# Kernel optimization log

Hardware: AMD Instinct MI355X
Metric: run time of the kernel (lower is better)

## Reference

```python
import jax, jax.numpy as jnp
import numpy as np

DIM = 128
HEADS = 32
DIM_HEAD = 64
INNER = DIM * DIM_HEAD  # 8192, as written in the source (dim * dim_head)
D = INNER // HEADS      # 256 per-head dim
B, N = 1, 2048
ROT = 64                # partial rotary width (l)
SCALE = DIM ** (-0.5)   # source uses dim**-0.5, not head-dim


def _rotate_half(x):
    # x: [..., l]; split as (j d) with j=2 -> cat(-x2, x1)
    x1, x2 = jnp.split(x, 2, axis=-1)
    return jnp.concatenate((-x2, x1), axis=-1)


def _apply_rotary(q, k, freqs):
    # freqs: [n, l]; q,k: [b,h,n,d] with l <= d (partial rotary)
    l = freqs.shape[-1]
    cos, sin = jnp.cos(freqs), jnp.sin(freqs)  # broadcast over b,h
    ql, qr = q[..., :l], q[..., l:]
    kl, kr = k[..., :l], k[..., l:]
    ql = ql * cos + _rotate_half(ql) * sin
    kl = kl * cos + _rotate_half(kl) * sin
    return jnp.concatenate((ql, qr), axis=-1), jnp.concatenate((kl, kr), axis=-1)


def setup_inputs() -> dict:
    key = jax.random.key(0)
    k1, k2, k3, k4, k5 = jax.random.split(key, 5)
    return {
        "x": jax.random.normal(k1, (B, N, DIM), dtype=jnp.float32),
        "Wqkv": jax.random.normal(k2, (3 * INNER, DIM), dtype=jnp.float32) * 0.02,
        "Wproj": jax.random.normal(k3, (DIM, INNER), dtype=jnp.float32) * 0.02,
        "bproj": jax.random.normal(k4, (DIM,), dtype=jnp.float32) * 0.02,
        "rotary_pos_emb": jax.random.normal(k5, (N, ROT), dtype=jnp.float32),
    }


def reference(x, Wqkv, Wproj, bproj, rotary_pos_emb):
    b, n, _ = x.shape
    qkv = x @ Wqkv.T                                   # [b, n, 3*inner]
    qkv = qkv.reshape(b, n, 3, HEADS, D)               # (qkv h d) ordering
    qkv = jnp.transpose(qkv, (2, 0, 3, 1, 4))          # [3, b, h, n, d]
    q, k, v = qkv[0], qkv[1], qkv[2]
    q, k = _apply_rotary(q, k, rotary_pos_emb)
    energy = jnp.einsum("bhid,bhjd->bhij", q, k) * SCALE  # [b,h,n,n]
    attn = jax.nn.softmax(energy, axis=-1)
    out = jnp.einsum("bhij,bhjd->bhid", attn, v)       # [b,h,n,d]
    out = jnp.transpose(out, (0, 2, 1, 3)).reshape(b, n, INNER)
    return out @ Wproj.T + bproj
```

## Files before the change

### kernel.cpp

```cpp
#include <hip/hip_runtime.h>


typedef unsigned short u16;
typedef unsigned int u32;
typedef __attribute__((ext_vector_type(8))) u16 u16x8;
typedef __attribute__((ext_vector_type(8))) __bf16 bf16x8;
typedef __attribute__((ext_vector_type(4))) float f32x4;
typedef __attribute__((ext_vector_type(16))) float f32x16;
typedef __attribute__((ext_vector_type(4))) u32 u32x4;
typedef __attribute__((ext_vector_type(2))) u32 u32x2;

#define DEV static __device__ __forceinline__

DEV u16 f2b(float f) {
  __bf16 h = (__bf16)f;
  return __builtin_bit_cast(u16, h);
}
DEV float b2f(u16 b) {
  u32 u = ((u32)b) << 16;
  return __builtin_bit_cast(float, u);
}
DEV u32 pk2(float a, float b) { return (u32)f2b(a) | ((u32)f2b(b) << 16); }

DEV f32x4 mfma16(u16x8 a, u16x8 b, f32x4 c) {
  return __builtin_amdgcn_mfma_f32_16x16x32_bf16(
      __builtin_bit_cast(bf16x8, a), __builtin_bit_cast(bf16x8, b), c, 0, 0, 0);
}
DEV f32x16 mfma32(u16x8 a, u16x8 b, f32x16 c) {
  return __builtin_amdgcn_mfma_f32_32x32x16_bf16(
      __builtin_bit_cast(bf16x8, a), __builtin_bit_cast(bf16x8, b), c, 0, 0, 0);
}

DEV int swz(int row, int kelem, int rowBytes) {
  return row * rowBytes + ((kelem * 2) ^ ((row & 7) << 4));
}

DEV void dma16(const void* g, void* l) {
  __builtin_amdgcn_global_load_lds(
      (const __attribute__((address_space(1))) void*)g,
      (__attribute__((address_space(3))) void*)l, 16, 0, 0);
}

__global__ __launch_bounds__(256) void k_cvt(const float* __restrict__ src,
                                             u16* __restrict__ dst, int n8) {
  int i = blockIdx.x * 256 + threadIdx.x;
  if (i >= n8) return;
  const float4* s = (const float4*)src;
  float4 a = s[i * 2], b = s[i * 2 + 1];
  u16x8 o;
  o[0] = f2b(a.x); o[1] = f2b(a.y); o[2] = f2b(a.z); o[3] = f2b(a.w);
  o[4] = f2b(b.x); o[5] = f2b(b.y); o[6] = f2b(b.z); o[7] = f2b(b.w);
  *(u16x8*)(dst + (size_t)i * 8) = o;
}

__global__ __launch_bounds__(256) void k_qkv(const u16* __restrict__ xb,
                                             const u16* __restrict__ wb,
                                             u16* __restrict__ qw,
                                             u16* __restrict__ kw,
                                             u16* __restrict__ vw) {
  __shared__ char lds[65536];
  const int tid = threadIdx.x;
  const int rt = blockIdx.x % 192, nt = blockIdx.x / 192;
  const int r0 = rt * 128, n0 = nt * 128;
#pragma unroll
  for (int p = 0; p < 8; ++p) {
    int row = p * 16 + (tid >> 4);
    int k0 = (tid & 15) * 8;
    *(u16x8*)(lds + swz(row, k0, 256)) =
        *(const u16x8*)(wb + (size_t)(r0 + row) * 128 + k0);
    *(u16x8*)(lds + 32768 + swz(row, k0, 256)) =
        *(const u16x8*)(xb + (size_t)(n0 + row) * 128 + k0);
  }
  __syncthreads();
  const int wid = tid >> 6, lane = tid & 63, lq = lane & 15, g = lane >> 4;
  const int wr = wid >> 1, wn = wid & 1;
  const bool isV = (r0 >= 16384);
  f32x4 acc[4][4] = {};
#pragma unroll
  for (int ks = 0; ks < 4; ++ks) {
    u16x8 wa[4], xa[4];
#pragma unroll
    for (int i = 0; i < 4; ++i) {
      int rw = wr * 64 + i * 16 + lq;
      wa[i] = *(const u16x8*)(lds + swz(rw, ks * 32 + g * 8, 256));
      int rx = wn * 64 + i * 16 + lq;
      xa[i] = *(const u16x8*)(lds + 32768 + swz(rx, ks * 32 + g * 8, 256));
    }
    if (!isV) {
#pragma unroll
      for (int i = 0; i < 4; ++i)
#pragma unroll
        for (int j = 0; j < 4; ++j) acc[i][j] = mfma16(wa[i], xa[j], acc[i][j]);
    } else {
#pragma unroll
      for (int i = 0; i < 4; ++i)
#pragma unroll
        for (int j = 0; j < 4; ++j) acc[i][j] = mfma16(xa[j], wa[i], acc[i][j]);
    }
  }
  const float SMQ = 0.08838834764831845f * 1.4426950408889634f;
  if (!isV) {
#pragma unroll
    for (int i = 0; i < 4; ++i) {
      int rb = r0 + wr * 64 + i * 16 + g * 4;
      u16* dst0 = (rb >= 8192) ? kw : qw;
      float scl = (rb >= 8192) ? 1.0f : SMQ;
      int hd = rb & 8191;
      int h = hd >> 8, db = hd & 255;
#pragma unroll
      for (int j = 0; j < 4; ++j) {
        int n = n0 + wn * 64 + j * 16 + lq;
        u32x2 pk;
        pk.x = pk2(acc[i][j][0] * scl, acc[i][j][1] * scl);
        pk.y = pk2(acc[i][j][2] * scl, acc[i][j][3] * scl);
        *(u32x2*)(dst0 + ((size_t)h * 2048 + n) * 256 + db) = pk;
      }
    }
  } else {
#pragma unroll
    for (int i = 0; i < 4; ++i) {
      int rc = r0 - 16384 + wr * 64 + i * 16 + lq;
      int h = rc >> 8, d = rc & 255;
#pragma unroll
      for (int j = 0; j < 4; ++j) {
        int nb = n0 + wn * 64 + j * 16 + g * 4;
        u32x2 pk;
        pk.x = pk2(acc[i][j][0], acc[i][j][1]);
        pk.y = pk2(acc[i][j][2], acc[i][j][3]);
        *(u32x2*)(vw + ((size_t)h * 256 + d) * 2048 + nb) = pk;
      }
    }
  }
}

__global__ __launch_bounds__(256) void k_rope(u16* __restrict__ qw,
                                              u16* __restrict__ kw,
                                              const float* __restrict__ fr) {
  int idx = blockIdx.x * 256 + threadIdx.x;
  int seg = idx & 3;
  int n = (idx >> 2) & 2047;
  int h = (idx >> 13) & 31;
  u16* base = ((idx >> 18) ? kw : qw) + ((size_t)h * 2048 + n) * 256 + seg * 8;
  u16x8 lo = *(const u16x8*)base;
  u16x8 hi = *(const u16x8*)(base + 32);
  const float* f = fr + n * 64 + seg * 8;
  u16x8 nlo, nhi;
#pragma unroll
  for (int e = 0; e < 8; ++e) {
    float fl = f[e], fh = f[e + 32];
    float sl, cl, sh, ch;
    __sincosf(fl, &sl, &cl);
    __sincosf(fh, &sh, &ch);
    float a = b2f(lo[e]), b = b2f(hi[e]);
    nlo[e] = f2b(a * cl - b * sl);
    nhi[e] = f2b(b * ch + a * sh);
  }
  *(u16x8*)base = nlo;
  *(u16x8*)(base + 32) = nhi;
}

__global__ __launch_bounds__(256, 2) void k_attn(const u16* __restrict__ qw,
                                                 const u16* __restrict__ kw,
                                                 const u16* __restrict__ vw,
                                                 u16* __restrict__ ow) {
  __shared__ char lds[65536];
  const int tid = threadIdx.x;
  const int h = blockIdx.x & 31;
  const int qb = blockIdx.x >> 5;
  const int wid = tid >> 6, lane = tid & 63;
  const int l31 = lane & 31, h2 = lane >> 5;
  const int q0w = qb * 128 + wid * 32;
  const int lane16 = lane * 16;

  const u16* kbase = kw + (size_t)h * 2048 * 256;
  const u16* vbase = vw + (size_t)h * 256 * 2048;

  int koff[4], voff[4];
  {
    int c0 = l31 & 3, hh = (l31 >> 2) & 1, c1 = l31 >> 3;
    int gkv = 16 * (c1 >> 1) + 8 * hh + 4 * (c1 & 1) + c0;
#pragma unroll
    for (int i = 0; i < 4; ++i) {
      int s = wid * 4 + i;
      koff[i] = gkv * 256 + s * 16 + h2 * 8;
      voff[i] = ((s >> 1) * 32 + l31) * 2048 + (s & 1) * 16 + h2 * 8;
    }
  }

  u16x8 qf[16];
  {
    const u16* qp = qw + ((size_t)h * 2048 + q0w + l31) * 256 + h2 * 8;
#pragma unroll
    for (int dt = 0; dt < 16; ++dt) qf[dt] = *(const u16x8*)(qp + dt * 16);
  }

  f32x16 oacc[8] = {};
  float lrun = 0.f;

#define STAGE(T, BUF)                                                 \
  {                                                                   \
    const int kv0_ = (T) * 32;                                        \
    char* b_ = lds + (BUF) * 32768;                                   \
    _Pragma("unroll") for (int i = 0; i < 4; ++i) {                   \
      dma16(kbase + (size_t)kv0_ * 256 + koff[i],                     \
            b_ + (wid * 4 + i) * 1024);                               \
      dma16(vbase + kv0_ + voff[i],                                   \
            b_ + 16384 + (wid * 4 + i) * 1024);                       \
    }                                                                 \
  }

  STAGE(0, 0);

  for (int t = 0; t < 64; ++t) {
    asm volatile("s_waitcnt vmcnt(0)" ::: "memory");
    __builtin_amdgcn_s_barrier();
    asm volatile("" ::: "memory");
    if (t < 63) STAGE(t + 1, (t + 1) & 1);

    const char* kb = lds + (t & 1) * 32768;

    f32x16 sA = {}, sB = {};
    __builtin_amdgcn_s_setprio(1);
#pragma unroll
    for (int dt = 0; dt < 16; dt += 2) {
      u16x8 ka0 = *(const u16x8*)(kb + dt * 1024 + lane16);
      sA = mfma32(ka0, qf[dt], sA);
      u16x8 ka1 = *(const u16x8*)(kb + (dt + 1) * 1024 + lane16);
      sB = mfma32(ka1, qf[dt + 1], sB);
    }
    __builtin_amdgcn_s_setprio(0);

    float p[16];
#pragma unroll
    for (int r = 0; r < 16; ++r)
      p[r] = __builtin_amdgcn_exp2f(sA[r] + sB[r]);
    float s8[8];
#pragma unroll
    for (int r = 0; r < 8; ++r) s8[r] = p[r] + p[r + 8];
#pragma unroll
    for (int r = 0; r < 4; ++r) s8[r] = s8[r] + s8[r + 4];
    lrun += (s8[0] + s8[1]) + (s8[2] + s8[3]);

    u32x4 b0v, b1v;
#pragma unroll
    for (int w = 0; w < 4; ++w) {
      b0v[w] = pk2(p[2 * w], p[2 * w + 1]);
      b1v[w] = pk2(p[8 + 2 * w], p[9 + 2 * w]);
    }
    u16x8 pb0 = __builtin_bit_cast(u16x8, b0v);
    u16x8 pb1 = __builtin_bit_cast(u16x8, b1v);

    const char* vb = kb + 16384;
    __builtin_amdgcn_s_setprio(1);
#pragma unroll
    for (int dt = 0; dt < 8; ++dt) {
      u16x8 v0 = *(const u16x8*)(vb + (dt * 2) * 1024 + lane16);
      oacc[dt] = mfma32(v0, pb0, oacc[dt]);
      u16x8 v1 = *(const u16x8*)(vb + (dt * 2 + 1) * 1024 + lane16);
      oacc[dt] = mfma32(v1, pb1, oacc[dt]);
    }
    __builtin_amdgcn_s_setprio(0);
  }
#undef STAGE

  lrun += __shfl_xor(lrun, 32);
  float inv = 1.0f / lrun;
  u16* orow = ow + (size_t)(q0w + l31) * 8192 + h * 256 + h2 * 4;
#pragma unroll
  for (int dt = 0; dt < 8; ++dt)
#pragma unroll
    for (int k = 0; k < 4; ++k) {
      u32x2 o2;
      o2.x = pk2(oacc[dt][4 * k] * inv, oacc[dt][4 * k + 1] * inv);
      o2.y = pk2(oacc[dt][4 * k + 2] * inv, oacc[dt][4 * k + 3] * inv);
      *(u32x2*)(orow + dt * 32 + k * 8) = o2;
    }
}

__global__ __launch_bounds__(256) void k_proj(const u16* __restrict__ ow,
                                              const u16* __restrict__ wp,
                                              float* __restrict__ part) {
  __shared__ char lds[49152];
  const int tid = threadIdx.x;
  const int nt = blockIdx.x >> 3, kc = blockIdx.x & 7;
  const int n0 = nt * 64, kb = kc * 1024;
  const int wid = tid >> 6, lane = tid & 63, lq = lane & 15, g = lane >> 4;
  f32x4 acc[8] = {};
  for (int kt = 0; kt < 8; ++kt) {
    int kk = kb + kt * 128;
#pragma unroll
    for (int p = 0; p < 4; ++p) {
      int nr = p * 16 + (tid >> 4);
      int k0 = (tid & 15) * 8;
      *(u16x8*)(lds + swz(nr, k0, 256)) =
          *(const u16x8*)(ow + (size_t)(n0 + nr) * 8192 + kk + k0);
    }
#pragma unroll
    for (int p = 0; p < 8; ++p) {
      int er = p * 16 + (tid >> 4);
      int k0 = (tid & 15) * 8;
      *(u16x8*)(lds + 16384 + swz(er, k0, 256)) =
          *(const u16x8*)(wp + (size_t)er * 8192 + kk + k0);
    }
    __syncthreads();
#pragma unroll
    for (int ks = 0; ks < 4; ++ks) {
      int nr = wid * 16 + lq;
      u16x8 oa = *(const u16x8*)(lds + swz(nr, ks * 32 + g * 8, 256));
#pragma unroll
      for (int ef = 0; ef < 8; ++ef) {
        int er = ef * 16 + lq;
        u16x8 wf = *(const u16x8*)(lds + 16384 + swz(er, ks * 32 + g * 8, 256));
        acc[ef] = mfma16(oa, wf, acc[ef]);
      }
    }
    __syncthreads();
  }
  float* pb = part + (size_t)kc * 262144;
#pragma unroll
  for (int ef = 0; ef < 8; ++ef)
#pragma unroll
    for (int r = 0; r < 4; ++r) {
      int n = n0 + wid * 16 + g * 4 + r;
      pb[n * 128 + ef * 16 + lq] = acc[ef][r];
    }
}

__global__ __launch_bounds__(256) void k_reduce(const float* __restrict__ part,
                                                const float* __restrict__ bias,
                                                float* __restrict__ out) {
  int i = blockIdx.x * 256 + threadIdx.x;
  float s = bias[i & 127];
#pragma unroll
  for (int c = 0; c < 8; ++c) s += part[(size_t)c * 262144 + i];
  out[i] = s;
}

extern "C" void kernel_launch(void* const* d_in, const int* in_sizes, int n_in,
                              void* d_out, int out_size, void* d_ws, size_t ws_size,
                              hipStream_t stream) {
  const float* x = (const float*)d_in[0];
  const float* wqkv = (const float*)d_in[1];
  const float* wproj = (const float*)d_in[2];
  const float* bproj = (const float*)d_in[3];
  const float* rope = (const float*)d_in[4];
  char* ws = (char*)d_ws;
  u16* xb    = (u16*)(ws);
  u16* wqkvb = (u16*)(ws + 524288);
  u16* wpb   = (u16*)(ws + 6815744);
  u16* qw    = (u16*)(ws + 8912896);
  u16* kw    = (u16*)(ws + 42467328);
  u16* vw    = (u16*)(ws + 76021760);
  u16* owv   = (u16*)(ws + 109576192);
  float* part = (float*)(ws + 8912896);

  k_cvt<<<128, 256, 0, stream>>>(x, xb, 32768);
  k_cvt<<<1536, 256, 0, stream>>>(wqkv, wqkvb, 393216);
  k_cvt<<<512, 256, 0, stream>>>(wproj, wpb, 131072);
  k_qkv<<<3072, 256, 0, stream>>>(xb, wqkvb, qw, kw, vw);
  k_rope<<<2048, 256, 0, stream>>>(qw, kw, rope);
  k_attn<<<512, 256, 0, stream>>>(qw, kw, vw, owv);
  k_proj<<<256, 256, 0, stream>>>(owv, wpb, part);
  k_reduce<<<1024, 256, 0, stream>>>(part, bproj, (float*)d_out);
}
```

Baseline: 240.4 us.

## Process two query tiles per wave in attention to reuse K/V fragments

Each wave now handles 64 query rows as two 32-row chunks, so every K and V fragment read from LDS feeds two MFMAs instead of one. The grid is halved to 256 blocks and launch bounds drop to one block per CU to allow the doubled Q and accumulator register footprint. The aim is to cut LDS reads and global K/V staging traffic per unit of compute. The cost is much higher register pressure and lower occupancy, and 256 blocks may underfill the 256 CUs' latency hiding.

```diff
diff --git a/kernel.cpp b/kernel.cpp
--- a/kernel.cpp
+++ b/kernel.cpp
@@ -159,7 +159,7 @@
   *(u16x8*)(base + 32) = nhi;
 }
 
-__global__ __launch_bounds__(256, 2) void k_attn(const u16* __restrict__ qw,
+__global__ __launch_bounds__(256, 1) void k_attn(const u16* __restrict__ qw,
                                                  const u16* __restrict__ kw,
                                                  const u16* __restrict__ vw,
                                                  u16* __restrict__ ow) {
@@ -169,7 +169,7 @@
   const int qb = blockIdx.x >> 5;
   const int wid = tid >> 6, lane = tid & 63;
   const int l31 = lane & 31, h2 = lane >> 5;
-  const int q0w = qb * 128 + wid * 32;
+  const int q0w = qb * 256 + wid * 64;
   const int lane16 = lane * 16;
 
   const u16* kbase = kw + (size_t)h * 2048 * 256;
@@ -187,15 +187,17 @@
     }
   }
 
-  u16x8 qf[16];
-  {
-    const u16* qp = qw + ((size_t)h * 2048 + q0w + l31) * 256 + h2 * 8;
-#pragma unroll
-    for (int dt = 0; dt < 16; ++dt) qf[dt] = *(const u16x8*)(qp + dt * 16);
-  }
-
-  f32x16 oacc[8] = {};
-  float lrun = 0.f;
+  u16x8 qf[2][16];
+#pragma unroll
+  for (int c = 0; c < 2; ++c) {
+    const u16* qp =
+        qw + ((size_t)h * 2048 + q0w + c * 32 + l31) * 256 + h2 * 8;
+#pragma unroll
+    for (int dt = 0; dt < 16; ++dt) qf[c][dt] = *(const u16x8*)(qp + dt * 16);
+  }
+
+  f32x16 oa0[8] = {}, oa1[8] = {};
+  float lrun0 = 0.f, lrun1 = 0.f;
 
 #define STAGE(T, BUF)                                                 \
   {                                                                   \
@@ -219,61 +221,88 @@
 
     const char* kb = lds + (t & 1) * 32768;
 
-    f32x16 sA = {}, sB = {};
+    f32x16 s0 = {}, s1 = {};
     __builtin_amdgcn_s_setprio(1);
 #pragma unroll
-    for (int dt = 0; dt < 16; dt += 2) {
-      u16x8 ka0 = *(const u16x8*)(kb + dt * 1024 + lane16);
-      sA = mfma32(ka0, qf[dt], sA);
-      u16x8 ka1 = *(const u16x8*)(kb + (dt + 1) * 1024 + lane16);
-      sB = mfma32(ka1, qf[dt + 1], sB);
+    for (int dt = 0; dt < 16; ++dt) {
+      u16x8 ka = *(const u16x8*)(kb + dt * 1024 + lane16);
+      s0 = mfma32(ka, qf[0][dt], s0);
+      s1 = mfma32(ka, qf[1][dt], s1);
     }
     __builtin_amdgcn_s_setprio(0);
 
-    float p[16];
-#pragma unroll
-    for (int r = 0; r < 16; ++r)
-      p[r] = __builtin_amdgcn_exp2f(sA[r] + sB[r]);
-    float s8[8];
-#pragma unroll
-    for (int r = 0; r < 8; ++r) s8[r] = p[r] + p[r + 8];
-#pragma unroll
-    for (int r = 0; r < 4; ++r) s8[r] = s8[r] + s8[r + 4];
-    lrun += (s8[0] + s8[1]) + (s8[2] + s8[3]);
-
-    u32x4 b0v, b1v;
-#pragma unroll
-    for (int w = 0; w < 4; ++w) {
-      b0v[w] = pk2(p[2 * w], p[2 * w + 1]);
-      b1v[w] = pk2(p[8 + 2 * w], p[9 + 2 * w]);
-    }
-    u16x8 pb0 = __builtin_bit_cast(u16x8, b0v);
-    u16x8 pb1 = __builtin_bit_cast(u16x8, b1v);
+    u16x8 pb00, pb01, pb10, pb11;
+    {
+      float p[16];
+#pragma unroll
+      for (int r = 0; r < 16; ++r) p[r] = __builtin_amdgcn_exp2f(s0[r]);
+      float t8[8];
+#pragma unroll
+      for (int r = 0; r < 8; ++r) t8[r] = p[r] + p[r + 8];
+#pragma unroll
+      for (int r = 0; r < 4; ++r) t8[r] = t8[r] + t8[r + 4];
+      lrun0 += (t8[0] + t8[1]) + (t8[2] + t8[3]);
+      u32x4 b0v, b1v;
+#pragma unroll
+      for (int w = 0; w < 4; ++w) {
+        b0v[w] = pk2(p[2 * w], p[2 * w + 1]);
+        b1v[w] = pk2(p[8 + 2 * w], p[9 + 2 * w]);
+      }
+      pb00 = __builtin_bit_cast(u16x8, b0v);
+      pb01 = __builtin_bit_cast(u16x8, b1v);
+    }
+    {
+      float p[16];
+#pragma unroll
+      for (int r = 0; r < 16; ++r) p[r] = __builtin_amdgcn_exp2f(s1[r]);
+      float t8[8];
+#pragma unroll
+      for (int r = 0; r < 8; ++r) t8[r] = p[r] + p[r + 8];
+#pragma unroll
+      for (int r = 0; r < 4; ++r) t8[r] = t8[r] + t8[r + 4];
+      lrun1 += (t8[0] + t8[1]) + (t8[2] + t8[3]);
+      u32x4 b0v, b1v;
+#pragma unroll
+      for (int w = 0; w < 4; ++w) {
+        b0v[w] = pk2(p[2 * w], p[2 * w + 1]);
+        b1v[w] = pk2(p[8 + 2 * w], p[9 + 2 * w]);
+      }
+      pb10 = __builtin_bit_cast(u16x8, b0v);
+      pb11 = __builtin_bit_cast(u16x8, b1v);
+    }
 
     const char* vb = kb + 16384;
     __builtin_amdgcn_s_setprio(1);
 #pragma unroll
     for (int dt = 0; dt < 8; ++dt) {
       u16x8 v0 = *(const u16x8*)(vb + (dt * 2) * 1024 + lane16);
-      oacc[dt] = mfma32(v0, pb0, oacc[dt]);
+      oa0[dt] = mfma32(v0, pb00, oa0[dt]);
+      oa1[dt] = mfma32(v0, pb10, oa1[dt]);
       u16x8 v1 = *(const u16x8*)(vb + (dt * 2 + 1) * 1024 + lane16);
-      oacc[dt] = mfma32(v1, pb1, oacc[dt]);
+      oa0[dt] = mfma32(v1, pb01, oa0[dt]);
+      oa1[dt] = mfma32(v1, pb11, oa1[dt]);
     }
     __builtin_amdgcn_s_setprio(0);
   }
 #undef STAGE
 
-  lrun += __shfl_xor(lrun, 32);
-  float inv = 1.0f / lrun;
-  u16* orow = ow + (size_t)(q0w + l31) * 8192 + h * 256 + h2 * 4;
+  lrun0 += __shfl_xor(lrun0, 32);
+  lrun1 += __shfl_xor(lrun1, 32);
+  float inv0 = 1.0f / lrun0, inv1 = 1.0f / lrun1;
+  u16* orow0 = ow + (size_t)(q0w + l31) * 8192 + h * 256 + h2 * 4;
+  u16* orow1 = orow0 + 32 * 8192;
 #pragma unroll
   for (int dt = 0; dt < 8; ++dt)
 #pragma unroll
     for (int k = 0; k < 4; ++k) {
       u32x2 o2;
-      o2.x = pk2(oacc[dt][4 * k] * inv, oacc[dt][4 * k + 1] * inv);
-      o2.y = pk2(oacc[dt][4 * k + 2] * inv, oacc[dt][4 * k + 3] * inv);
-      *(u32x2*)(orow + dt * 32 + k * 8) = o2;
+      o2.x = pk2(oa0[dt][4 * k] * inv0, oa0[dt][4 * k + 1] * inv0);
+      o2.y = pk2(oa0[dt][4 * k + 2] * inv0, oa0[dt][4 * k + 3] * inv0);
+      *(u32x2*)(orow0 + dt * 32 + k * 8) = o2;
+      u32x2 o3;
+      o3.x = pk2(oa1[dt][4 * k] * inv1, oa1[dt][4 * k + 1] * inv1);
+      o3.y = pk2(oa1[dt][4 * k + 2] * inv1, oa1[dt][4 * k + 3] * inv1);
+      *(u32x2*)(orow1 + dt * 32 + k * 8) = o3;
     }
 }
 
@@ -359,7 +388,7 @@
   k_cvt<<<512, 256, 0, stream>>>(wproj, wpb, 131072);
   k_qkv<<<3072, 256, 0, stream>>>(xb, wqkvb, qw, kw, vw);
   k_rope<<<2048, 256, 0, stream>>>(qw, kw, rope);
-  k_attn<<<512, 256, 0, stream>>>(qw, kw, vw, owv);
+  k_attn<<<256, 256, 0, stream>>>(qw, kw, vw, owv);
   k_proj<<<256, 256, 0, stream>>>(owv, wpb, part);
   k_reduce<<<1024, 256, 0, stream>>>(part, bproj, (float*)d_out);
 }
```

Result: faster. 231.0 us (-3.9%).

## Load V directly from global into registers and merge conversion launches

Applied to the files above, without the earlier changes.

In the attention kernel, V tiles are no longer staged through LDS by DMA. Each lane now loads its V operand fragments straight from global memory into registers at the start of each KV step, which halves the LDS footprint (32 KB) and may allow more blocks per CU. The three fp32-to-bf16 conversion kernels are merged into a single launch that picks its source by index range. The risk is that the direct V loads sit on the critical path, get only partial overlap with the QK MFMAs, and add register pressure with 16 extra vector registers' worth of operands.

```diff
diff --git a/kernel.cpp b/kernel.cpp
--- a/kernel.cpp
+++ b/kernel.cpp
@@ -41,10 +41,22 @@
       (__attribute__((address_space(3))) void*)l, 16, 0, 0);
 }
 
-__global__ __launch_bounds__(256) void k_cvt(const float* __restrict__ src,
-                                             u16* __restrict__ dst, int n8) {
+__global__ __launch_bounds__(256) void k_cvt3(const float* __restrict__ s0,
+                                              u16* __restrict__ d0,
+                                              const float* __restrict__ s1,
+                                              u16* __restrict__ d1,
+                                              const float* __restrict__ s2,
+                                              u16* __restrict__ d2) {
   int i = blockIdx.x * 256 + threadIdx.x;
-  if (i >= n8) return;
+  const float* src;
+  u16* dst;
+  if (i < 32768) {
+    src = s0; dst = d0;
+  } else if (i < 425984) {
+    src = s1; dst = d1; i -= 32768;
+  } else {
+    src = s2; dst = d2; i -= 425984;
+  }
   const float4* s = (const float4*)src;
   float4 a = s[i * 2], b = s[i * 2 + 1];
   u16x8 o;
@@ -163,7 +175,7 @@
                                                  const u16* __restrict__ kw,
                                                  const u16* __restrict__ vw,
                                                  u16* __restrict__ ow) {
-  __shared__ char lds[65536];
+  __shared__ char lds[32768];
   const int tid = threadIdx.x;
   const int h = blockIdx.x & 31;
   const int qb = blockIdx.x >> 5;
@@ -175,7 +187,7 @@
   const u16* kbase = kw + (size_t)h * 2048 * 256;
   const u16* vbase = vw + (size_t)h * 256 * 2048;
 
-  int koff[4], voff[4];
+  int koff[4];
   {
     int c0 = l31 & 3, hh = (l31 >> 2) & 1, c1 = l31 >> 3;
     int gkv = 16 * (c1 >> 1) + 8 * hh + 4 * (c1 & 1) + c0;
@@ -183,9 +195,13 @@
     for (int i = 0; i < 4; ++i) {
       int s = wid * 4 + i;
       koff[i] = gkv * 256 + s * 16 + h2 * 8;
-      voff[i] = ((s >> 1) * 32 + l31) * 2048 + (s & 1) * 16 + h2 * 8;
-    }
-  }
+    }
+  }
+
+  int voffs[8];
+#pragma unroll
+  for (int dt = 0; dt < 8; ++dt)
+    voffs[dt] = ((dt * 32 + l31) * 2048 + h2 * 8) * 2;
 
   u16x8 qf[16];
   {
@@ -200,12 +216,10 @@
 #define STAGE(T, BUF)                                                 \
   {                                                                   \
     const int kv0_ = (T) * 32;                                        \
-    char* b_ = lds + (BUF) * 32768;                                   \
+    char* b_ = lds + (BUF) * 16384;                                   \
     _Pragma("unroll") for (int i = 0; i < 4; ++i) {                   \
       dma16(kbase + (size_t)kv0_ * 256 + koff[i],                     \
             b_ + (wid * 4 + i) * 1024);                               \
-      dma16(vbase + kv0_ + voff[i],                                   \
-            b_ + 16384 + (wid * 4 + i) * 1024);                       \
     }                                                                 \
   }
 
@@ -215,9 +229,18 @@
     asm volatile("s_waitcnt vmcnt(0)" ::: "memory");
     __builtin_amdgcn_s_barrier();
     asm volatile("" ::: "memory");
+
+    const char* vB = (const char*)vbase + t * 64;
+    u16x8 va[16];
+#pragma unroll
+    for (int dt = 0; dt < 8; ++dt) {
+      va[2 * dt] = *(const u16x8*)(vB + voffs[dt]);
+      va[2 * dt + 1] = *(const u16x8*)(vB + voffs[dt] + 32);
+    }
+
     if (t < 63) STAGE(t + 1, (t + 1) & 1);
 
-    const char* kb = lds + (t & 1) * 32768;
+    const char* kb = lds + (t & 1) * 16384;
 
     f32x16 sA = {}, sB = {};
     __builtin_amdgcn_s_setprio(1);
@@ -250,14 +273,11 @@
     u16x8 pb0 = __builtin_bit_cast(u16x8, b0v);
     u16x8 pb1 = __builtin_bit_cast(u16x8, b1v);
 
-    const char* vb = kb + 16384;
     __builtin_amdgcn_s_setprio(1);
 #pragma unroll
     for (int dt = 0; dt < 8; ++dt) {
-      u16x8 v0 = *(const u16x8*)(vb + (dt * 2) * 1024 + lane16);
-      oacc[dt] = mfma32(v0, pb0, oacc[dt]);
-      u16x8 v1 = *(const u16x8*)(vb + (dt * 2 + 1) * 1024 + lane16);
-      oacc[dt] = mfma32(v1, pb1, oacc[dt]);
+      oacc[dt] = mfma32(va[2 * dt], pb0, oacc[dt]);
+      oacc[dt] = mfma32(va[2 * dt + 1], pb1, oacc[dt]);
     }
     __builtin_amdgcn_s_setprio(0);
   }
@@ -354,9 +374,7 @@
   u16* owv   = (u16*)(ws + 109576192);
   float* part = (float*)(ws + 8912896);
 
-  k_cvt<<<128, 256, 0, stream>>>(x, xb, 32768);
-  k_cvt<<<1536, 256, 0, stream>>>(wqkv, wqkvb, 393216);
-  k_cvt<<<512, 256, 0, stream>>>(wproj, wpb, 131072);
+  k_cvt3<<<2176, 256, 0, stream>>>(x, xb, wqkv, wqkvb, wproj, wpb);
   k_qkv<<<3072, 256, 0, stream>>>(xb, wqkvb, qw, kw, vw);
   k_rope<<<2048, 256, 0, stream>>>(qw, kw, rope);
   k_attn<<<512, 256, 0, stream>>>(qw, kw, vw, owv);
```

Result: slower. 696.5 us (+189.8%).
